# Kernel optimization log

Measured on AMD Instinct MI355X. Metric: run time of the kernel, lower is better.

## Reference

```python
import jax, jax.numpy as jnp
import numpy as np

N_NODES = 1_000_000
N_EDGES = 32_000_000


def setup_inputs() -> dict:
    key = jax.random.key(0)
    k1, k2, k3, k4, k5 = jax.random.split(key, 5)
    state = jax.random.normal(k1, (N_NODES, 1), dtype=jnp.float32)
    edge_src = jax.random.randint(k2, (N_EDGES,), 0, N_NODES, dtype=jnp.int64)
    edge_dst = jax.random.randint(k3, (N_EDGES,), 0, N_NODES, dtype=jnp.int64)
    W = jax.random.normal(k4, (1, 2), dtype=jnp.float32)
    b = jax.random.normal(k5, (1,), dtype=jnp.float32)
    return {"state": state, "edge_src": edge_src, "edge_dst": edge_dst, "W": W, "b": b}


def reference(state, edge_src, edge_dst, W, b):
    # neighbor_sum[dst] += state[src]  (irregular gather + scatter-add)
    n = state.shape[0]
    messages = state[edge_src, 0]                              # [E]
    neighbor_sum = jax.ops.segment_sum(messages, edge_dst, num_segments=n)  # [n]
    x = jnp.concatenate([state, neighbor_sum[:, None]], axis=1)  # [n, 2]
    return x @ W.T + b                                           # [n, 1]
```

## Files before the change

### kernel.cpp

```cpp
#include <hip/hip_runtime.h>
#include <hip/hip_fp16.h>


#define NB_SHIFT 14
#define RANGE    (1 << NB_SHIFT)
#define NBALL    64
#define TPB      1024
#define IPT      8
#define TILE     (TPB * IPT)
#define GSPLIT   8

typedef int   iv4 __attribute__((ext_vector_type(4)));
typedef float fv4 __attribute__((ext_vector_type(4)));

__global__ void k_init_cursors(int* __restrict__ cursors) {
    if (threadIdx.x < NBALL) cursors[threadIdx.x] = 0;
}

__global__ __launch_bounds__(TPB) void k_partition(
    const float* __restrict__ state,
    const int* __restrict__ src,
    const int* __restrict__ dst,
    unsigned* __restrict__ records,
    int* __restrict__ cursors,
    int n_edges, int cap)
{
    __shared__ unsigned stage[TILE];
    __shared__ int cnt[NBALL];
    __shared__ int sbase[NBALL];
    __shared__ int gbase[NBALL];

    const int tid = threadIdx.x;
    if (tid < NBALL) cnt[tid] = 0;

    const long long e0 = (long long)blockIdx.x * TILE + (long long)tid * IPT;

    unsigned rec[IPT];
    int bk[IPT];
    int pos[IPT];

    if (e0 + IPT <= (long long)n_edges) {
        const long long i4 = e0 >> 2;
        iv4 sA = __builtin_nontemporal_load((const iv4*)src + i4);
        iv4 sB = __builtin_nontemporal_load((const iv4*)src + i4 + 1);
        iv4 dA = __builtin_nontemporal_load((const iv4*)dst + i4);
        iv4 dB = __builtin_nontemporal_load((const iv4*)dst + i4 + 1);
        int s[IPT] = { sA[0], sA[1], sA[2], sA[3], sB[0], sB[1], sB[2], sB[3] };
        int d[IPT] = { dA[0], dA[1], dA[2], dA[3], dB[0], dB[1], dB[2], dB[3] };
        float v[IPT];
        #pragma unroll
        for (int k = 0; k < IPT; ++k) v[k] = state[s[k]];
        #pragma unroll
        for (int k = 0; k < IPT; ++k) {
            unsigned hb = (unsigned)__half_as_ushort(__float2half_rn(v[k]));
            bk[k]  = d[k] >> NB_SHIFT;
            rec[k] = (hb << NB_SHIFT) | (unsigned)(d[k] & (RANGE - 1));
        }
    } else {
        #pragma unroll
        for (int k = 0; k < IPT; ++k) {
            long long e = e0 + k;
            if (e < n_edges) {
                int s = src[e];
                int d = dst[e];
                unsigned hb = (unsigned)__half_as_ushort(__float2half_rn(state[s]));
                bk[k]  = d >> NB_SHIFT;
                rec[k] = (hb << NB_SHIFT) | (unsigned)(d & (RANGE - 1));
            } else {
                bk[k] = -1; rec[k] = 0;
            }
        }
    }
    __syncthreads();

    #pragma unroll
    for (int k = 0; k < IPT; ++k)
        if (bk[k] >= 0) pos[k] = atomicAdd(&cnt[bk[k]], 1);
    __syncthreads();

    if (tid < NBALL) {
        int h = cnt[tid];
        int v = h;
        #pragma unroll
        for (int off = 1; off < 64; off <<= 1) {
            int u = __shfl_up(v, off);
            if (tid >= off) v += u;
        }
        sbase[tid] = v - h;
        gbase[tid] = atomicAdd(&cursors[tid], h);
    }
    __syncthreads();

    #pragma unroll
    for (int k = 0; k < IPT; ++k)
        if (bk[k] >= 0) stage[sbase[bk[k]] + pos[k]] = rec[k];
    __syncthreads();

    const int total = sbase[NBALL - 1] + cnt[NBALL - 1];
    for (int j = tid; j < total; j += TPB) {
        unsigned r = stage[j];
        int b = 0;
        #pragma unroll
        for (int s = 32; s; s >>= 1)
            if (b + s < NBALL && sbase[b + s] <= j) b += s;
        int gpos = gbase[b] + (j - sbase[b]);
        __builtin_nontemporal_store(r, &records[(size_t)b * cap + gpos]);
    }
}

__global__ __launch_bounds__(TPB) void k_bins(
    const unsigned* __restrict__ records,
    const int* __restrict__ cursors,
    float* __restrict__ partial,
    int cap)
{
    __shared__ float bins[RANGE];
    const int b = blockIdx.x / GSPLIT;
    const int g = blockIdx.x % GSPLIT;
    const int cnt = cursors[b];
    const size_t base = (size_t)b * cap;
    const int lo = (int)((long long)cnt * g       / GSPLIT);
    const int hi = (int)((long long)cnt * (g + 1) / GSPLIT);

    for (int i = threadIdx.x; i < RANGE; i += TPB) bins[i] = 0.0f;
    __syncthreads();

    for (int i = lo + threadIdx.x; i < hi; i += TPB) {
        unsigned r = __builtin_nontemporal_load(&records[base + i]);
        float v = __half2float(__ushort_as_half((unsigned short)(r >> NB_SHIFT)));
        atomicAdd(&bins[r & (RANGE - 1)], v);
    }
    __syncthreads();

    float* p = partial + (size_t)blockIdx.x * RANGE;
    for (int i = threadIdx.x; i < RANGE; i += TPB)
        __builtin_nontemporal_store(bins[i], &p[i]);
}

__global__ __launch_bounds__(256) void k_finalize(
    const float* __restrict__ state,
    const float* __restrict__ partial,
    const float* __restrict__ W,
    const float* __restrict__ bias,
    float* __restrict__ out, int n)
{
    const int i = (blockIdx.x * blockDim.x + threadIdx.x) * 4;
    if (i >= n) return;
    const int b   = i >> NB_SHIFT;
    const int loc = i & (RANGE - 1);
    const float* pb = partial + (size_t)b * GSPLIT * RANGE + loc;
    fv4 s = {0.f, 0.f, 0.f, 0.f};
    #pragma unroll
    for (int g = 0; g < GSPLIT; ++g) {
        fv4 t = __builtin_nontemporal_load((const fv4*)(pb + (size_t)g * RANGE));
        s += t;
    }
    const float w0 = W[0], w1 = W[1], bb = bias[0];
    fv4 st = *(const fv4*)(state + i);
    fv4 o;
    #pragma unroll
    for (int k = 0; k < 4; ++k) o[k] = fmaf(st[k], w0, fmaf(s[k], w1, bb));
    *(fv4*)(out + i) = o;
}

__global__ __launch_bounds__(256) void gnn_zero(float4* __restrict__ ws, int n4) {
    int i = blockIdx.x * blockDim.x + threadIdx.x;
    int stride = gridDim.x * blockDim.x;
    const float4 z = make_float4(0.f, 0.f, 0.f, 0.f);
    for (; i < n4; i += stride) ws[i] = z;
}

__global__ __launch_bounds__(256) void gnn_scatter_dev(const float* __restrict__ state,
                                                       const int* __restrict__ src,
                                                       const int* __restrict__ dst,
                                                       float* __restrict__ nsum,
                                                       int n_edges) {
    const int tid = blockIdx.x * blockDim.x + threadIdx.x;
    const int stride = gridDim.x * blockDim.x;
    const int n4 = n_edges >> 2;
    const int4* __restrict__ src4 = (const int4*)src;
    const int4* __restrict__ dst4 = (const int4*)dst;
    for (int i = tid; i < n4; i += stride) {
        int4 s = src4[i];
        int4 d = dst4[i];
        atomicAdd(&nsum[d.x], state[s.x]);
        atomicAdd(&nsum[d.y], state[s.y]);
        atomicAdd(&nsum[d.z], state[s.z]);
        atomicAdd(&nsum[d.w], state[s.w]);
    }
    for (int i = (n4 << 2) + tid; i < n_edges; i += stride)
        atomicAdd(&nsum[dst[i]], state[src[i]]);
}

__global__ __launch_bounds__(256) void gnn_finalize_flat(const float* __restrict__ state,
                                                         const float* __restrict__ nsum,
                                                         const float* __restrict__ W,
                                                         const float* __restrict__ b,
                                                         float* __restrict__ out, int n) {
    int i = blockIdx.x * blockDim.x + threadIdx.x;
    if (i < n) out[i] = fmaf(state[i], W[0], fmaf(nsum[i], W[1], b[0]));
}

extern "C" void kernel_launch(void* const* d_in, const int* in_sizes, int n_in,
                              void* d_out, int out_size, void* d_ws, size_t ws_size,
                              hipStream_t stream) {
    const float* state = (const float*)d_in[0];
    const int*   esrc  = (const int*)d_in[1];
    const int*   edst  = (const int*)d_in[2];
    const float* W     = (const float*)d_in[3];
    const float* b     = (const float*)d_in[4];
    float* out = (float*)d_out;

    const int n_nodes = in_sizes[0];
    const int n_edges = in_sizes[1];

    const int nbused = (n_nodes + RANGE - 1) >> NB_SHIFT;
    const long long lam = (long long)n_edges * RANGE / n_nodes;
    const int cap = (int)(lam + lam / 16 + 1024);

    const size_t recBytes = (size_t)nbused * cap * sizeof(unsigned);
    const size_t curOff   = (recBytes + 255) & ~(size_t)255;
    const size_t parOff   = curOff + ((NBALL * sizeof(int) + 255) & ~(size_t)255);
    const size_t parBytes = (size_t)nbused * GSPLIT * RANGE * sizeof(float);
    const size_t need     = parOff + parBytes;

    if (ws_size >= need && (n_nodes & 3) == 0 && (n_edges & 3) == 0) {
        unsigned* records = (unsigned*)d_ws;
        int*      cursors = (int*)((char*)d_ws + curOff);
        float*    partial = (float*)((char*)d_ws + parOff);

        k_init_cursors<<<1, NBALL, 0, stream>>>(cursors);

        int tiles = (n_edges + TILE - 1) / TILE;
        k_partition<<<tiles, TPB, 0, stream>>>(state, esrc, edst,
                                               records, cursors, n_edges, cap);

        k_bins<<<nbused * GSPLIT, TPB, 0, stream>>>(records, cursors, partial, cap);

        int blocks = (n_nodes / 4 + 255) / 256;
        k_finalize<<<blocks, 256, 0, stream>>>(state, partial, W, b, out, n_nodes);
    } else {
        float* nsum = (float*)d_ws;
        int n4n = n_nodes >> 2;
        int zb = (n4n + 255) / 256; if (zb > 2048) zb = 2048;
        gnn_zero<<<zb, 256, 0, stream>>>((float4*)nsum, n4n);
        int work = n_edges >> 2;
        int sb = (work + 255) / 256; if (sb > 8192) sb = 8192;
        gnn_scatter_dev<<<sb, 256, 0, stream>>>(state, esrc, edst, nsum, n_edges);
        int fb = (n_nodes + 255) / 256;
        gnn_finalize_flat<<<fb, 256, 0, stream>>>(state, nsum, W, b, out, n_nodes);
    }
}
```

Before: 411.1 us.

## Pre-convert state to fp16, replicate bucket cursors, per-wave bucket flush

Adds a pre-pass that converts the state to a 2-byte half array, so the random gather in the partition kernel touches half the bytes and the conversion leaves the hot loop. Each bucket gets four replica cursors and regions chosen by block index, to reduce contention on the global atomics. The partition tile is halved to 512 threads, and the flush now gives each wave whole buckets instead of binary-searching per element. The bin kernel reads records as 4-wide vectors. The cost is an extra kernel launch, a different workspace layout, and per-replica capacity slack (lamR/8) that could overflow if bucket counts vary more than expected.

```diff
diff --git a/kernel.cpp b/kernel.cpp
--- a/kernel.cpp
+++ b/kernel.cpp
@@ -5,25 +5,42 @@
 #define NB_SHIFT 14
 #define RANGE    (1 << NB_SHIFT)
 #define NBALL    64
-#define TPB      1024
+#define TPB      512
 #define IPT      8
 #define TILE     (TPB * IPT)
-#define GSPLIT   8
+#define NWAVES   (TPB / 64)
+#define NREP     4
+#define GSPL     2
+#define BPB      (NREP * GSPL)
 
 typedef int   iv4 __attribute__((ext_vector_type(4)));
 typedef float fv4 __attribute__((ext_vector_type(4)));
+typedef unsigned uv4 __attribute__((ext_vector_type(4)));
 
 __global__ void k_init_cursors(int* __restrict__ cursors) {
-    if (threadIdx.x < NBALL) cursors[threadIdx.x] = 0;
+    cursors[threadIdx.x] = 0;
+}
+
+__global__ __launch_bounds__(256) void k_cvt(const float* __restrict__ state,
+                                             unsigned short* __restrict__ sh, int n4) {
+    int i = blockIdx.x * blockDim.x + threadIdx.x;
+    if (i >= n4) return;
+    fv4 v = *(const fv4*)(state + i * 4);
+    ushort4 h;
+    h.x = __half_as_ushort(__float2half_rn(v[0]));
+    h.y = __half_as_ushort(__float2half_rn(v[1]));
+    h.z = __half_as_ushort(__float2half_rn(v[2]));
+    h.w = __half_as_ushort(__float2half_rn(v[3]));
+    *(ushort4*)(sh + i * 4) = h;
 }
 
 __global__ __launch_bounds__(TPB) void k_partition(
-    const float* __restrict__ state,
+    const unsigned short* __restrict__ sh,
     const int* __restrict__ src,
     const int* __restrict__ dst,
     unsigned* __restrict__ records,
     int* __restrict__ cursors,
-    int n_edges, int cap)
+    int n_edges, int capR)
 {
     __shared__ unsigned stage[TILE];
     __shared__ int cnt[NBALL];
@@ -31,6 +48,7 @@
     __shared__ int gbase[NBALL];
 
     const int tid = threadIdx.x;
+    const int rep = blockIdx.x & (NREP - 1);
     if (tid < NBALL) cnt[tid] = 0;
 
     const long long e0 = (long long)blockIdx.x * TILE + (long long)tid * IPT;
@@ -47,25 +65,23 @@
         iv4 dB = __builtin_nontemporal_load((const iv4*)dst + i4 + 1);
         int s[IPT] = { sA[0], sA[1], sA[2], sA[3], sB[0], sB[1], sB[2], sB[3] };
         int d[IPT] = { dA[0], dA[1], dA[2], dA[3], dB[0], dB[1], dB[2], dB[3] };
-        float v[IPT];
-        #pragma unroll
-        for (int k = 0; k < IPT; ++k) v[k] = state[s[k]];
+        unsigned v[IPT];
+        #pragma unroll
+        for (int k = 0; k < IPT; ++k) v[k] = sh[s[k]];
         #pragma unroll
         for (int k = 0; k < IPT; ++k) {
-            unsigned hb = (unsigned)__half_as_ushort(__float2half_rn(v[k]));
             bk[k]  = d[k] >> NB_SHIFT;
-            rec[k] = (hb << NB_SHIFT) | (unsigned)(d[k] & (RANGE - 1));
+            rec[k] = (v[k] << NB_SHIFT) | (unsigned)(d[k] & (RANGE - 1));
         }
     } else {
         #pragma unroll
         for (int k = 0; k < IPT; ++k) {
             long long e = e0 + k;
             if (e < n_edges) {
-                int s = src[e];
                 int d = dst[e];
-                unsigned hb = (unsigned)__half_as_ushort(__float2half_rn(state[s]));
+                unsigned v = sh[src[e]];
                 bk[k]  = d >> NB_SHIFT;
-                rec[k] = (hb << NB_SHIFT) | (unsigned)(d & (RANGE - 1));
+                rec[k] = (v << NB_SHIFT) | (unsigned)(d & (RANGE - 1));
             } else {
                 bk[k] = -1; rec[k] = 0;
             }
@@ -87,7 +103,7 @@
             if (tid >= off) v += u;
         }
         sbase[tid] = v - h;
-        gbase[tid] = atomicAdd(&cursors[tid], h);
+        gbase[tid] = atomicAdd(&cursors[(tid << 2) | rep], h);
     }
     __syncthreads();
 
@@ -96,45 +112,53 @@
         if (bk[k] >= 0) stage[sbase[bk[k]] + pos[k]] = rec[k];
     __syncthreads();
 
-    const int total = sbase[NBALL - 1] + cnt[NBALL - 1];
-    for (int j = tid; j < total; j += TPB) {
-        unsigned r = stage[j];
-        int b = 0;
-        #pragma unroll
-        for (int s = 32; s; s >>= 1)
-            if (b + s < NBALL && sbase[b + s] <= j) b += s;
-        int gpos = gbase[b] + (j - sbase[b]);
-        __builtin_nontemporal_store(r, &records[(size_t)b * cap + gpos]);
-    }
-}
-
-__global__ __launch_bounds__(TPB) void k_bins(
+    const int wid = tid >> 6, lane = tid & 63;
+    for (int b = wid; b < NBALL; b += NWAVES) {
+        const int sb = sbase[b], h = cnt[b], gb = gbase[b];
+        unsigned* dstp = records + (size_t)((b << 2) | rep) * capR + gb;
+        for (int j = lane; j < h; j += 64)
+            __builtin_nontemporal_store(stage[sb + j], dstp + j);
+    }
+}
+
+__global__ __launch_bounds__(1024) void k_bins(
     const unsigned* __restrict__ records,
     const int* __restrict__ cursors,
     float* __restrict__ partial,
-    int cap)
+    int capR)
 {
     __shared__ float bins[RANGE];
-    const int b = blockIdx.x / GSPLIT;
-    const int g = blockIdx.x % GSPLIT;
-    const int cnt = cursors[b];
-    const size_t base = (size_t)b * cap;
-    const int lo = (int)((long long)cnt * g       / GSPLIT);
-    const int hi = (int)((long long)cnt * (g + 1) / GSPLIT);
-
-    for (int i = threadIdx.x; i < RANGE; i += TPB) bins[i] = 0.0f;
-    __syncthreads();
-
-    for (int i = lo + threadIdx.x; i < hi; i += TPB) {
-        unsigned r = __builtin_nontemporal_load(&records[base + i]);
+    const int b   = blockIdx.x / BPB;
+    const int sub = blockIdx.x % BPB;
+    const int rep = sub >> 1;
+    const int g   = sub & 1;
+    const int cnt = cursors[(b << 2) | rep];
+    const size_t base = (size_t)((b << 2) | rep) * capR;
+    const int lo = (int)((long long)cnt * g       / GSPL);
+    const int hi = (int)((long long)cnt * (g + 1) / GSPL);
+
+    for (int i = threadIdx.x; i < RANGE; i += 1024) bins[i] = 0.0f;
+    __syncthreads();
+
+    int i = lo + threadIdx.x * 4;
+    for (; i + 4 <= hi; i += 1024 * 4) {
+        uv4 r = __builtin_nontemporal_load((const uv4*)(records + base + i));
+        #pragma unroll
+        for (int k = 0; k < 4; ++k) {
+            float v = __half2float(__ushort_as_half((unsigned short)(r[k] >> NB_SHIFT)));
+            atomicAdd(&bins[r[k] & (RANGE - 1)], v);
+        }
+    }
+    for (int j = lo + ((hi - lo) & ~3) + (int)threadIdx.x; j < hi; j += 1024) {
+        unsigned r = __builtin_nontemporal_load(&records[base + j]);
         float v = __half2float(__ushort_as_half((unsigned short)(r >> NB_SHIFT)));
         atomicAdd(&bins[r & (RANGE - 1)], v);
     }
     __syncthreads();
 
     float* p = partial + (size_t)blockIdx.x * RANGE;
-    for (int i = threadIdx.x; i < RANGE; i += TPB)
-        __builtin_nontemporal_store(bins[i], &p[i]);
+    for (int i2 = threadIdx.x; i2 < RANGE; i2 += 1024)
+        __builtin_nontemporal_store(bins[i2], &p[i2]);
 }
 
 __global__ __launch_bounds__(256) void k_finalize(
@@ -148,13 +172,11 @@
     if (i >= n) return;
     const int b   = i >> NB_SHIFT;
     const int loc = i & (RANGE - 1);
-    const float* pb = partial + (size_t)b * GSPLIT * RANGE + loc;
+    const float* pb = partial + (size_t)b * BPB * RANGE + loc;
     fv4 s = {0.f, 0.f, 0.f, 0.f};
     #pragma unroll
-    for (int g = 0; g < GSPLIT; ++g) {
-        fv4 t = __builtin_nontemporal_load((const fv4*)(pb + (size_t)g * RANGE));
-        s += t;
-    }
+    for (int g = 0; g < BPB; ++g)
+        s += __builtin_nontemporal_load((const fv4*)(pb + (size_t)g * RANGE));
     const float w0 = W[0], w1 = W[1], bb = bias[0];
     fv4 st = *(const fv4*)(state + i);
     fv4 o;
@@ -215,27 +237,33 @@
     const int n_edges = in_sizes[1];
 
     const int nbused = (n_nodes + RANGE - 1) >> NB_SHIFT;
-    const long long lam = (long long)n_edges * RANGE / n_nodes;
-    const int cap = (int)(lam + lam / 16 + 1024);
-
-    const size_t recBytes = (size_t)nbused * cap * sizeof(unsigned);
-    const size_t curOff   = (recBytes + 255) & ~(size_t)255;
-    const size_t parOff   = curOff + ((NBALL * sizeof(int) + 255) & ~(size_t)255);
-    const size_t parBytes = (size_t)nbused * GSPLIT * RANGE * sizeof(float);
-    const size_t need     = parOff + parBytes;
+    const long long lamR = (long long)n_edges * RANGE / n_nodes / NREP;
+    const int capR = (int)(lamR + lamR / 8 + 1024);
+
+    const size_t shOff   = 0;
+    const size_t shBytes = ((size_t)n_nodes * 2 + 255) & ~(size_t)255;
+    const size_t recOff  = shBytes;
+    const size_t recBytes= ((size_t)NBALL * NREP * capR * 4 + 255) & ~(size_t)255;
+    const size_t curOff  = recOff + recBytes;
+    const size_t curBytes= (256 * sizeof(int) + 255) & ~(size_t)255;
+    const size_t parOff  = curOff + curBytes;
+    const size_t parBytes= (size_t)nbused * BPB * RANGE * sizeof(float);
+    const size_t need    = parOff + parBytes;
 
     if (ws_size >= need && (n_nodes & 3) == 0 && (n_edges & 3) == 0) {
-        unsigned* records = (unsigned*)d_ws;
-        int*      cursors = (int*)((char*)d_ws + curOff);
-        float*    partial = (float*)((char*)d_ws + parOff);
-
-        k_init_cursors<<<1, NBALL, 0, stream>>>(cursors);
+        unsigned short* sh = (unsigned short*)((char*)d_ws + shOff);
+        unsigned* records  = (unsigned*)((char*)d_ws + recOff);
+        int*      cursors  = (int*)((char*)d_ws + curOff);
+        float*    partial  = (float*)((char*)d_ws + parOff);
+
+        k_init_cursors<<<1, 256, 0, stream>>>(cursors);
+        k_cvt<<<(n_nodes / 4 + 255) / 256, 256, 0, stream>>>(state, sh, n_nodes / 4);
 
         int tiles = (n_edges + TILE - 1) / TILE;
-        k_partition<<<tiles, TPB, 0, stream>>>(state, esrc, edst,
-                                               records, cursors, n_edges, cap);
-
-        k_bins<<<nbused * GSPLIT, TPB, 0, stream>>>(records, cursors, partial, cap);
+        k_partition<<<tiles, TPB, 0, stream>>>(sh, esrc, edst,
+                                               records, cursors, n_edges, capR);
+
+        k_bins<<<nbused * BPB, 1024, 0, stream>>>(records, cursors, partial, capR);
 
         int blocks = (n_nodes / 4 + 255) / 256;
         k_finalize<<<blocks, 256, 0, stream>>>(state, partial, W, b, out, n_nodes);
```

New measurement: 386.6 us. 6.0% less time.
